# Kernel tuning notes

Measured on AMD Instinct MI355X. Metric: run time of the kernel, lower is better.

## Reference

```python
import jax, jax.numpy as jnp
import numpy as np

D_MODEL = 256
N_HEAD = 8


def quick_gelu(x):
    return x * jax.nn.sigmoid(1.702 * x)


def setup_inputs() -> dict:
    key = jax.random.key(0)
    ks = jax.random.split(key, 7)
    d = D_MODEL
    s = 0.02
    return {
        "x": jax.random.normal(ks[0], (2, 512, d), dtype=jnp.float32),
        "W_qkv": jax.random.normal(ks[1], (d, 3 * d), dtype=jnp.float32) * s,
        "b_qkv": jnp.zeros((3 * d,), dtype=jnp.float32),
        "W_fc": jax.random.normal(ks[2], (d, 4 * d), dtype=jnp.float32) * s,
        "b_fc": jnp.zeros((4 * d,), dtype=jnp.float32),
        "W_proj": jax.random.normal(ks[3], (4 * d, d), dtype=jnp.float32) * s,
        "b_proj": jnp.zeros((d,), dtype=jnp.float32),
    }


def attention_l1(x, W_qkv, b_qkv):
    bs, n_ctx, width = x.shape
    h = N_HEAD
    c = width // h
    scale = 1.0 / jnp.sqrt(jnp.asarray(c, x.dtype))
    qkv = (x @ W_qkv + b_qkv).reshape(bs, n_ctx, h, 3 * c)
    q, k, v = jnp.split(qkv, 3, axis=-1)  # each (b, t, h, c)
    qh = q.transpose(0, 2, 1, 3)  # (b, h, t, c)
    kh = k.transpose(0, 2, 1, 3)  # (b, h, s, c)
    vh = v.transpose(0, 2, 1, 3)  # (b, h, s, c)
    # L1 distance: sum_c |q - k| * scale  -> (b, h, t, s)
    dist = jnp.sum(jnp.abs(qh[:, :, :, None, :] - kh[:, :, None, :, :]), axis=-1) * scale
    weight = 1.0 / (0.001 + dist)
    idx = jnp.arange(n_ctx)
    weight = weight.at[:, :, idx, idx].set(0.0)
    wdtype = weight.dtype
    weight = jax.nn.softmax(weight.astype(jnp.float32), axis=-1).astype(wdtype)
    out = jnp.einsum('bhts,bhsc->bthc', weight, vh)
    return out.reshape(bs, n_ctx, width)


def reference(x, W_qkv, b_qkv, W_fc, b_fc, W_proj, b_proj):
    x = x + attention_l1(x, W_qkv, b_qkv)
    h = quick_gelu(x @ W_fc + b_fc)
    x = x + (h @ W_proj + b_proj)
    return x
```

## Files before the change

kernel.cpp:

```cpp
#include <hip/hip_runtime.h>
#include <hip/hip_bf16.h>
#include <hip/hip_fp16.h>

#define DM   256
#define NH   8
#define HC   32
#define SEQ  512
#define MTOT 1024

#define B_X1   0
#define B_QH   (1u<<20)
#define B_KH   0x180000u
#define B_VT   0x200000u
#define B_WFCT 0x280000u
#define B_WPJT 0x300000u

typedef __attribute__((ext_vector_type(8))) __bf16 bf16x8;
typedef __attribute__((ext_vector_type(4))) __bf16 bf16x4;
typedef __attribute__((ext_vector_type(4))) float  f32x4;

__device__ __forceinline__ float qgelu(float x) {
    return x / (1.0f + __expf(-1.702f * x));
}

__global__ __launch_bounds__(256)
void qkv_k(const float* __restrict__ x, const float* __restrict__ W,
           const float* __restrict__ bias,
           const float* __restrict__ Wfc, const float* __restrict__ Wproj,
           char* __restrict__ wsb)
{
    __shared__ float lt[64 * 65];
    const int bid = blockIdx.x, tid = threadIdx.x;

    if (bid >= 768) {
        const int tt = bid - 768;
        const float* src; __bf16* dst; int K, N, tile;
        if (tt < 64) { src = Wfc;   dst = (__bf16*)(wsb + B_WFCT); K = 256;  N = 1024; tile = tt; }
        else         { src = Wproj; dst = (__bf16*)(wsb + B_WPJT); K = 1024; N = 256;  tile = tt - 64; }
        const int nn = N >> 6;
        const int k0 = (tile / nn) * 64, n0 = (tile % nn) * 64;
        const int rr0 = tid >> 4, c4 = tid & 15;
        #pragma unroll
        for (int i = 0; i < 4; ++i) {
            const int rr = rr0 + i * 16;
            float4 v = *(const float4*)&src[(size_t)(k0 + rr) * N + n0 + c4 * 4];
            lt[rr * 65 + c4 * 4 + 0] = v.x; lt[rr * 65 + c4 * 4 + 1] = v.y;
            lt[rr * 65 + c4 * 4 + 2] = v.z; lt[rr * 65 + c4 * 4 + 3] = v.w;
        }
        __syncthreads();
        #pragma unroll
        for (int i = 0; i < 4; ++i) {
            const int rr = rr0 + i * 16;
            bf16x4 b;
            b.x = (__bf16)lt[(c4 * 4 + 0) * 65 + rr];
            b.y = (__bf16)lt[(c4 * 4 + 1) * 65 + rr];
            b.z = (__bf16)lt[(c4 * 4 + 2) * 65 + rr];
            b.w = (__bf16)lt[(c4 * 4 + 3) * 65 + rr];
            *(bf16x4*)&dst[(size_t)(n0 + rr) * K + k0 + c4 * 4] = b;
        }
        return;
    }

    const int lane = tid & 63, wv = tid >> 6;
    const int widx = bid * 4 + wv;
    const int m0 = (widx & 63) * 16, n0 = (widx >> 6) * 16;
    const int r = lane & 15, q = lane >> 4;

    const float* ap = x + (size_t)(m0 + r) * DM + q * 8;
    const float* bp = W + (size_t)(q * 8) * 768 + n0 + r;

    f32x4 acc = {0.f, 0.f, 0.f, 0.f};
    #pragma unroll
    for (int kt = 0; kt < DM; kt += 32) {
        float4 a0 = *(const float4*)(ap + kt);
        float4 a1 = *(const float4*)(ap + kt + 4);
        bf16x8 af;
        af[0] = (__bf16)a0.x; af[1] = (__bf16)a0.y; af[2] = (__bf16)a0.z; af[3] = (__bf16)a0.w;
        af[4] = (__bf16)a1.x; af[5] = (__bf16)a1.y; af[6] = (__bf16)a1.z; af[7] = (__bf16)a1.w;
        bf16x8 bf;
        #pragma unroll
        for (int j = 0; j < 8; ++j)
            bf[j] = (__bf16)bp[(size_t)(kt + j) * 768];
        acc = __builtin_amdgcn_mfma_f32_16x16x32_bf16(af, bf, acc, 0, 0, 0);
    }

    __half*  qh  = (__half*)(wsb + B_QH);
    __half*  kh  = (__half*)(wsb + B_KH);
    __bf16*  vtb = (__bf16*)(wsb + B_VT);
    const int n = n0 + r;
    const float bn = bias[n];
    const int h = n / 96, jj = n % 96;
    #pragma unroll
    for (int i = 0; i < 4; ++i) {
        const int m = m0 + q * 4 + i;
        const float v = acc[i] + bn;
        const int b = m >> 9, t = m & 511;
        const int bh = b * NH + h;
        if (jj < 32)      qh[((size_t)(bh * SEQ + t)) * HC + jj]        = (__half)v;
        else if (jj < 64) kh[((size_t)(bh * SEQ + t)) * HC + (jj - 32)] = (__half)v;
        else              vtb[((size_t)(bh * HC + (jj - 64))) * SEQ + t] = (__bf16)v;
    }
}

#define QT 16
#define PSTRIDE 514

__global__ __launch_bounds__(512, 4)
void attn_k(const char* __restrict__ wsb, const float* __restrict__ xin,
            float* __restrict__ x1, const float* __restrict__ bproj,
            float* __restrict__ out)
{
    __shared__ __half2 qtile[QT * 16];
    __shared__ __bf16  pmat[QT * PSTRIDE];
    __shared__ float   psum[QT * 8];
    __shared__ float   pinv[QT];

    const __half*  qhg = (const __half*)(wsb + B_QH);
    const __half*  khg = (const __half*)(wsb + B_KH);
    const __bf16*  vtb = (const __bf16*)(wsb + B_VT);

    const int tid  = threadIdx.x;
    const int lane = tid & 63;
    const int wv   = tid >> 6;
    const int sg   = tid;
    const int bh   = blockIdx.x >> 5;
    const int qbase = (blockIdx.x & 31) * QT;
    const float scale = 0.17677669529663687f;

    const __half2* kp = (const __half2*)(khg + ((size_t)(bh * SEQ + sg)) * HC);
    __half2 kr[16];
    #pragma unroll
    for (int j = 0; j < 16; ++j) kr[j] = kp[j];

    if (tid < 256) {
        const int t = tid >> 4, j = tid & 15;
        qtile[t * 16 + j] =
            *(const __half2*)(qhg + ((size_t)(bh * SEQ + qbase + t)) * HC + j * 2);
    }
    __syncthreads();

    #pragma unroll 4
    for (int t = 0; t < QT; ++t) {
        __half2 acc2 = __floats2half2_rn(0.f, 0.f);
        #pragma unroll
        for (int j = 0; j < 16; ++j) {
            __half2 dif = __hsub2(kr[j], qtile[t * 16 + j]);
            unsigned u = (*(unsigned*)&dif) & 0x7FFF7FFFu;
            acc2 = __hadd2(acc2, *(__half2*)&u);
        }
        const float d = __low2float(acc2) + __high2float(acc2);
        float w = 1.0f / (0.001f + d * scale);
        if (sg == qbase + t) w = 0.0f;
        float p = __expf(w);
        float se = p;
        #pragma unroll
        for (int off = 32; off >= 1; off >>= 1) se += __shfl_xor(se, off, 64);
        pmat[t * PSTRIDE + sg] = (__bf16)p;
        if (lane == 0) psum[t * 8 + wv] = se;
    }
    __syncthreads();

    if (tid < QT) {
        float s = 0.f;
        #pragma unroll
        for (int j = 0; j < 8; ++j) s += psum[tid * 8 + j];
        pinv[tid] = 1.0f / s;
    }
    __syncthreads();

    if (wv < 2) {
        const int r = lane & 15, q = lane >> 4;
        const __bf16* bp  = vtb + ((size_t)(bh * HC + wv * 16 + r)) * SEQ + q * 8;
        const __bf16* apm = &pmat[r * PSTRIDE + q * 8];
        f32x4 acc = {0.f, 0.f, 0.f, 0.f};
        #pragma unroll
        for (int kt = 0; kt < SEQ; kt += 32) {
            bf16x8 af = *(const bf16x8*)(apm + kt);
            bf16x8 bf = *(const bf16x8*)(bp + kt);
            acc = __builtin_amdgcn_mfma_f32_16x16x32_bf16(af, bf, acc, 0, 0, 0);
        }
        const int b = bh >> 3, hh = bh & 7;
        const int c = wv * 16 + r;
        const int col = hh * HC + c;
        const float bpn = bproj[col];
        #pragma unroll
        for (int i = 0; i < 4; ++i) {
            const int tl = q * 4 + i;
            const int t  = qbase + tl;
            const float v = acc[i] * pinv[tl];
            const int idx = ((b * SEQ + t) * DM) + col;
            const float res = xin[idx] + v;
            x1[idx]  = res;
            out[idx] = res + bpn;
        }
    }
}

#define HSTR 264

__global__ __launch_bounds__(256)
void mlp_k(const float* __restrict__ X1, const char* __restrict__ wsb,
           const float* __restrict__ bfc, float* __restrict__ out)
{
    __shared__ __bf16 hs[16 * HSTR];
    const __bf16* Wf = (const __bf16*)(wsb + B_WFCT);
    const __bf16* Wp = (const __bf16*)(wsb + B_WPJT);

    const int tid  = threadIdx.x;
    const int lane = tid & 63;
    const int wv   = tid >> 6;
    const int mt   = blockIdx.x & 63;
    const int ns   = blockIdx.x >> 6;
    const int m0   = mt * 16;
    const int r    = lane & 15, q = lane >> 4;

    {
        const float* ap = X1 + (size_t)(m0 + r) * DM + q * 8;
        f32x4 acc[4] = {};
        #pragma unroll
        for (int kt = 0; kt < DM; kt += 32) {
            float4 a0 = *(const float4*)(ap + kt);
            float4 a1 = *(const float4*)(ap + kt + 4);
            bf16x8 af;
            af[0] = (__bf16)a0.x; af[1] = (__bf16)a0.y; af[2] = (__bf16)a0.z; af[3] = (__bf16)a0.w;
            af[4] = (__bf16)a1.x; af[5] = (__bf16)a1.y; af[6] = (__bf16)a1.z; af[7] = (__bf16)a1.w;
            #pragma unroll
            for (int nt = 0; nt < 4; ++nt) {
                const int n0 = ns * 256 + (wv * 4 + nt) * 16;
                bf16x8 bf = *(const bf16x8*)(Wf + (size_t)(n0 + r) * DM + q * 8 + kt);
                acc[nt] = __builtin_amdgcn_mfma_f32_16x16x32_bf16(af, bf, acc[nt], 0, 0, 0);
            }
        }
        #pragma unroll
        for (int nt = 0; nt < 4; ++nt) {
            const int nl = (wv * 4 + nt) * 16 + r;
            const float bn = bfc[ns * 256 + nl];
            #pragma unroll
            for (int i = 0; i < 4; ++i)
                hs[(q * 4 + i) * HSTR + nl] = (__bf16)qgelu(acc[nt][i] + bn);
        }
    }
    __syncthreads();

    {
        f32x4 acc[4] = {};
        const __bf16* al = &hs[r * HSTR + q * 8];
        #pragma unroll
        for (int kt = 0; kt < 256; kt += 32) {
            bf16x8 af = *(const bf16x8*)(al + kt);
            #pragma unroll
            for (int nt = 0; nt < 4; ++nt) {
                const int n0 = wv * 64 + nt * 16;
                bf16x8 bf = *(const bf16x8*)(Wp + (size_t)(n0 + r) * 1024 +
                                             ns * 256 + q * 8 + kt);
                acc[nt] = __builtin_amdgcn_mfma_f32_16x16x32_bf16(af, bf, acc[nt], 0, 0, 0);
            }
        }
        #pragma unroll
        for (int nt = 0; nt < 4; ++nt) {
            const int n = wv * 64 + nt * 16 + r;
            #pragma unroll
            for (int i = 0; i < 4; ++i) {
                const int m = m0 + q * 4 + i;
                atomicAdd(&out[(size_t)m * DM + n], acc[nt][i]);
            }
        }
    }
}

extern "C" void kernel_launch(void* const* d_in, const int* in_sizes, int n_in,
                              void* d_out, int out_size, void* d_ws, size_t ws_size,
                              hipStream_t stream)
{
    (void)in_sizes; (void)n_in; (void)out_size; (void)ws_size;
    const float* x     = (const float*)d_in[0];
    const float* Wqkv  = (const float*)d_in[1];
    const float* bqkv  = (const float*)d_in[2];
    const float* Wfc   = (const float*)d_in[3];
    const float* bfc   = (const float*)d_in[4];
    const float* Wproj = (const float*)d_in[5];
    const float* bproj = (const float*)d_in[6];
    float* out = (float*)d_out;
    char*  wsb = (char*)d_ws;
    float* x1  = (float*)(wsb + B_X1);

    qkv_k<<<896, 256, 0, stream>>>(x, Wqkv, bqkv, Wfc, Wproj, wsb);

    attn_k<<<512, 512, 0, stream>>>(wsb, x, x1, bproj, out);

    mlp_k<<<256, 256, 0, stream>>>(x1, wsb, bfc, out);
}
```

Before: 106.3 us.

## Move weight transposes into attention kernel, store x1 as bf16, split L1 accumulators

Moves the Wfc/Wproj fp32-to-bf16 transpose blocks out of the QKV kernel and into extra blocks of the attention launch, so the conversion overlaps attention work instead of lengthening the QKV pass. The residual x1 is now written as bf16, which halves that write and the MLP's read and removes the in-kernel conversion. The L1 distance loop uses two independent half2 accumulators to shorten the dependency chain. Attention launch bounds drop from 4 to 2 blocks per CU, and the added 16.6KB lt buffer raises shared memory per block, so occupancy and register allocation may change.

```diff
diff --git a/kernel.cpp b/kernel.cpp
--- a/kernel.cpp
+++ b/kernel.cpp
@@ -8,7 +8,7 @@
 #define SEQ  512
 #define MTOT 1024
 
-#define B_X1   0
+#define B_X1B  0
 #define B_QH   (1u<<20)
 #define B_KH   0x180000u
 #define B_VT   0x200000u
@@ -25,44 +25,11 @@
 
 __global__ __launch_bounds__(256)
 void qkv_k(const float* __restrict__ x, const float* __restrict__ W,
-           const float* __restrict__ bias,
-           const float* __restrict__ Wfc, const float* __restrict__ Wproj,
-           char* __restrict__ wsb)
-{
-    __shared__ float lt[64 * 65];
-    const int bid = blockIdx.x, tid = threadIdx.x;
-
-    if (bid >= 768) {
-        const int tt = bid - 768;
-        const float* src; __bf16* dst; int K, N, tile;
-        if (tt < 64) { src = Wfc;   dst = (__bf16*)(wsb + B_WFCT); K = 256;  N = 1024; tile = tt; }
-        else         { src = Wproj; dst = (__bf16*)(wsb + B_WPJT); K = 1024; N = 256;  tile = tt - 64; }
-        const int nn = N >> 6;
-        const int k0 = (tile / nn) * 64, n0 = (tile % nn) * 64;
-        const int rr0 = tid >> 4, c4 = tid & 15;
-        #pragma unroll
-        for (int i = 0; i < 4; ++i) {
-            const int rr = rr0 + i * 16;
-            float4 v = *(const float4*)&src[(size_t)(k0 + rr) * N + n0 + c4 * 4];
-            lt[rr * 65 + c4 * 4 + 0] = v.x; lt[rr * 65 + c4 * 4 + 1] = v.y;
-            lt[rr * 65 + c4 * 4 + 2] = v.z; lt[rr * 65 + c4 * 4 + 3] = v.w;
-        }
-        __syncthreads();
-        #pragma unroll
-        for (int i = 0; i < 4; ++i) {
-            const int rr = rr0 + i * 16;
-            bf16x4 b;
-            b.x = (__bf16)lt[(c4 * 4 + 0) * 65 + rr];
-            b.y = (__bf16)lt[(c4 * 4 + 1) * 65 + rr];
-            b.z = (__bf16)lt[(c4 * 4 + 2) * 65 + rr];
-            b.w = (__bf16)lt[(c4 * 4 + 3) * 65 + rr];
-            *(bf16x4*)&dst[(size_t)(n0 + rr) * K + k0 + c4 * 4] = b;
-        }
-        return;
-    }
-
+           const float* __restrict__ bias, char* __restrict__ wsb)
+{
+    const int tid = threadIdx.x;
     const int lane = tid & 63, wv = tid >> 6;
-    const int widx = bid * 4 + wv;
+    const int widx = blockIdx.x * 4 + wv;
     const int m0 = (widx & 63) * 16, n0 = (widx >> 6) * 16;
     const int r = lane & 15, q = lane >> 4;
 
@@ -105,21 +72,56 @@
 #define QT 16
 #define PSTRIDE 514
 
-__global__ __launch_bounds__(512, 4)
-void attn_k(const char* __restrict__ wsb, const float* __restrict__ xin,
-            float* __restrict__ x1, const float* __restrict__ bproj,
-            float* __restrict__ out)
+__global__ __launch_bounds__(512, 2)
+void attn_k(const char* __restrict__ wsb_c, const float* __restrict__ xin,
+            const float* __restrict__ bproj, float* __restrict__ out,
+            const float* __restrict__ Wfc, const float* __restrict__ Wproj)
 {
     __shared__ __half2 qtile[QT * 16];
     __shared__ __bf16  pmat[QT * PSTRIDE];
     __shared__ float   psum[QT * 8];
     __shared__ float   pinv[QT];
+    __shared__ float   lt[64 * 65];
+
+    char* wsb = (char*)wsb_c;
+    const int tid = threadIdx.x;
+
+    if (blockIdx.x >= 512) {
+        const int tt = blockIdx.x - 512;
+        const float* src; __bf16* dst; int K, N, tile;
+        if (tt < 64) { src = Wfc;   dst = (__bf16*)(wsb + B_WFCT); K = 256;  N = 1024; tile = tt; }
+        else         { src = Wproj; dst = (__bf16*)(wsb + B_WPJT); K = 1024; N = 256;  tile = tt - 64; }
+        const int nn = N >> 6;
+        const int k0 = (tile / nn) * 64, n0 = (tile % nn) * 64;
+        const int rr = tid >> 3;
+        const int c4 = (tid & 7) * 2;
+        #pragma unroll
+        for (int p = 0; p < 2; ++p) {
+            float4 v = *(const float4*)&src[(size_t)(k0 + rr) * N + n0 + (c4 + p) * 4];
+            lt[rr * 65 + (c4 + p) * 4 + 0] = v.x;
+            lt[rr * 65 + (c4 + p) * 4 + 1] = v.y;
+            lt[rr * 65 + (c4 + p) * 4 + 2] = v.z;
+            lt[rr * 65 + (c4 + p) * 4 + 3] = v.w;
+        }
+        __syncthreads();
+        #pragma unroll
+        for (int p = 0; p < 2; ++p) {
+            const int kc = (c4 + p) * 4;
+            bf16x4 b;
+            b.x = (__bf16)lt[(kc + 0) * 65 + rr];
+            b.y = (__bf16)lt[(kc + 1) * 65 + rr];
+            b.z = (__bf16)lt[(kc + 2) * 65 + rr];
+            b.w = (__bf16)lt[(kc + 3) * 65 + rr];
+            *(bf16x4*)&dst[(size_t)(n0 + rr) * K + k0 + kc] = b;
+        }
+        return;
+    }
 
     const __half*  qhg = (const __half*)(wsb + B_QH);
     const __half*  khg = (const __half*)(wsb + B_KH);
     const __bf16*  vtb = (const __bf16*)(wsb + B_VT);
-
-    const int tid  = threadIdx.x;
+    __bf16*        x1b = (__bf16*)(wsb + B_X1B);
+
     const int lane = tid & 63;
     const int wv   = tid >> 6;
     const int sg   = tid;
@@ -141,13 +143,17 @@
 
     #pragma unroll 4
     for (int t = 0; t < QT; ++t) {
-        __half2 acc2 = __floats2half2_rn(0.f, 0.f);
-        #pragma unroll
-        for (int j = 0; j < 16; ++j) {
-            __half2 dif = __hsub2(kr[j], qtile[t * 16 + j]);
-            unsigned u = (*(unsigned*)&dif) & 0x7FFF7FFFu;
-            acc2 = __hadd2(acc2, *(__half2*)&u);
-        }
+        __half2 a0 = __floats2half2_rn(0.f, 0.f), a1 = a0;
+        #pragma unroll
+        for (int j = 0; j < 16; j += 2) {
+            __half2 d0 = __hsub2(kr[j],   qtile[t * 16 + j]);
+            __half2 d1 = __hsub2(kr[j+1], qtile[t * 16 + j + 1]);
+            unsigned u0 = (*(unsigned*)&d0) & 0x7FFF7FFFu;
+            unsigned u1 = (*(unsigned*)&d1) & 0x7FFF7FFFu;
+            a0 = __hadd2(a0, *(__half2*)&u0);
+            a1 = __hadd2(a1, *(__half2*)&u1);
+        }
+        __half2 acc2 = __hadd2(a0, a1);
         const float d = __low2float(acc2) + __high2float(acc2);
         float w = 1.0f / (0.001f + d * scale);
         if (sg == qbase + t) w = 0.0f;
@@ -190,7 +196,7 @@
             const float v = acc[i] * pinv[tl];
             const int idx = ((b * SEQ + t) * DM) + col;
             const float res = xin[idx] + v;
-            x1[idx]  = res;
+            x1b[idx] = (__bf16)res;
             out[idx] = res + bpn;
         }
     }
@@ -199,12 +205,13 @@
 #define HSTR 264
 
 __global__ __launch_bounds__(256)
-void mlp_k(const float* __restrict__ X1, const char* __restrict__ wsb,
-           const float* __restrict__ bfc, float* __restrict__ out)
+void mlp_k(const char* __restrict__ wsb, const float* __restrict__ bfc,
+           float* __restrict__ out)
 {
     __shared__ __bf16 hs[16 * HSTR];
-    const __bf16* Wf = (const __bf16*)(wsb + B_WFCT);
-    const __bf16* Wp = (const __bf16*)(wsb + B_WPJT);
+    const __bf16* X1B = (const __bf16*)(wsb + B_X1B);
+    const __bf16* Wf  = (const __bf16*)(wsb + B_WFCT);
+    const __bf16* Wp  = (const __bf16*)(wsb + B_WPJT);
 
     const int tid  = threadIdx.x;
     const int lane = tid & 63;
@@ -215,15 +222,11 @@
     const int r    = lane & 15, q = lane >> 4;
 
     {
-        const float* ap = X1 + (size_t)(m0 + r) * DM + q * 8;
+        const __bf16* ap = X1B + (size_t)(m0 + r) * DM + q * 8;
         f32x4 acc[4] = {};
         #pragma unroll
         for (int kt = 0; kt < DM; kt += 32) {
-            float4 a0 = *(const float4*)(ap + kt);
-            float4 a1 = *(const float4*)(ap + kt + 4);
-            bf16x8 af;
-            af[0] = (__bf16)a0.x; af[1] = (__bf16)a0.y; af[2] = (__bf16)a0.z; af[3] = (__bf16)a0.w;
-            af[4] = (__bf16)a1.x; af[5] = (__bf16)a1.y; af[6] = (__bf16)a1.z; af[7] = (__bf16)a1.w;
+            bf16x8 af = *(const bf16x8*)(ap + kt);
             #pragma unroll
             for (int nt = 0; nt < 4; ++nt) {
                 const int n0 = ns * 256 + (wv * 4 + nt) * 16;
@@ -282,11 +285,10 @@
     const float* bproj = (const float*)d_in[6];
     float* out = (float*)d_out;
     char*  wsb = (char*)d_ws;
-    float* x1  = (float*)(wsb + B_X1);
-
-    qkv_k<<<896, 256, 0, stream>>>(x, Wqkv, bqkv, Wfc, Wproj, wsb);
-
-    attn_k<<<512, 512, 0, stream>>>(wsb, x, x1, bproj, out);
-
-    mlp_k<<<256, 256, 0, stream>>>(x1, wsb, bfc, out);
-}
+
+    qkv_k<<<768, 256, 0, stream>>>(x, Wqkv, bqkv, wsb);
+
+    attn_k<<<640, 512, 0, stream>>>(wsb, x, bproj, out, Wfc, Wproj);
+
+    mlp_k<<<256, 256, 0, stream>>>(wsb, bfc, out);
+}
```

New measurement: 106.8 us. Within noise of the previous version (+0.5%).

## Fuse attention and MLP kernels with global counter barrier and bf16 x1

Applied to the files above, without the earlier changes.

Merges the attention and MLP launches into one grid of 768 blocks. The last 256 blocks spin on a global atomic counter until all 512 attention blocks have published their results. The intermediate x1 is now stored as bf16, which halves its traffic, and the MLP blocks move to 512 threads, each wave handling 2 N-tiles instead of 4. The aim is to drop one launch gap and overlap the MLP startup. The cost is that spinning blocks hold CU slots, there is a deadlock risk if the attention blocks cannot all become resident, the bounded spin loop can exit early, and the launch bounds drop to 2 blocks per CU.

```diff
diff --git a/kernel.cpp b/kernel.cpp
--- a/kernel.cpp
+++ b/kernel.cpp
@@ -8,12 +8,13 @@
 #define SEQ  512
 #define MTOT 1024
 
-#define B_X1   0
+#define B_X1B  0
 #define B_QH   (1u<<20)
 #define B_KH   0x180000u
 #define B_VT   0x200000u
 #define B_WFCT 0x280000u
 #define B_WPJT 0x300000u
+#define B_CTR  0x380000u
 
 typedef __attribute__((ext_vector_type(8))) __bf16 bf16x8;
 typedef __attribute__((ext_vector_type(4))) __bf16 bf16x4;
@@ -31,6 +32,8 @@
 {
     __shared__ float lt[64 * 65];
     const int bid = blockIdx.x, tid = threadIdx.x;
+
+    if (bid == 0 && tid == 0) *(unsigned*)(wsb + B_CTR) = 0u;
 
     if (bid >= 768) {
         const int tt = bid - 768;
@@ -104,136 +107,151 @@
 
 #define QT 16
 #define PSTRIDE 514
-
-__global__ __launch_bounds__(512, 4)
-void attn_k(const char* __restrict__ wsb, const float* __restrict__ xin,
-            float* __restrict__ x1, const float* __restrict__ bproj,
-            float* __restrict__ out)
+#define HSTR 264
+
+__global__ __launch_bounds__(512, 2)
+void attn_mlp_k(char* __restrict__ wsb, const float* __restrict__ xin,
+                const float* __restrict__ bproj, const float* __restrict__ bfc,
+                float* __restrict__ out)
 {
-    __shared__ __half2 qtile[QT * 16];
-    __shared__ __bf16  pmat[QT * PSTRIDE];
-    __shared__ float   psum[QT * 8];
-    __shared__ float   pinv[QT];
-
-    const __half*  qhg = (const __half*)(wsb + B_QH);
-    const __half*  khg = (const __half*)(wsb + B_KH);
-    const __bf16*  vtb = (const __bf16*)(wsb + B_VT);
-
-    const int tid  = threadIdx.x;
+    __shared__ __align__(16) char smem[18048];
+    unsigned* ctr = (unsigned*)(wsb + B_CTR);
+    const int tid = threadIdx.x;
     const int lane = tid & 63;
     const int wv   = tid >> 6;
-    const int sg   = tid;
-    const int bh   = blockIdx.x >> 5;
-    const int qbase = (blockIdx.x & 31) * QT;
-    const float scale = 0.17677669529663687f;
-
-    const __half2* kp = (const __half2*)(khg + ((size_t)(bh * SEQ + sg)) * HC);
-    __half2 kr[16];
-    #pragma unroll
-    for (int j = 0; j < 16; ++j) kr[j] = kp[j];
-
-    if (tid < 256) {
-        const int t = tid >> 4, j = tid & 15;
-        qtile[t * 16 + j] =
-            *(const __half2*)(qhg + ((size_t)(bh * SEQ + qbase + t)) * HC + j * 2);
+
+    if (blockIdx.x < 512) {
+        __bf16*  pmat  = (__bf16*)smem;
+        __half2* qtile = (__half2*)(smem + 16448);
+        float*   psum  = (float*)(smem + 17472);
+        float*   pinv  = (float*)(smem + 17984);
+
+        const __half* qhg = (const __half*)(wsb + B_QH);
+        const __half* khg = (const __half*)(wsb + B_KH);
+        const __bf16* vtb = (const __bf16*)(wsb + B_VT);
+        __bf16*       x1b = (__bf16*)(wsb + B_X1B);
+
+        const int sg   = tid;
+        const int bh   = blockIdx.x >> 5;
+        const int qbase = (blockIdx.x & 31) * QT;
+        const float scale = 0.17677669529663687f;
+
+        const __half2* kp = (const __half2*)(khg + ((size_t)(bh * SEQ + sg)) * HC);
+        __half2 kr[16];
+        #pragma unroll
+        for (int j = 0; j < 16; ++j) kr[j] = kp[j];
+
+        if (tid < 256) {
+            const int t = tid >> 4, j = tid & 15;
+            qtile[t * 16 + j] =
+                *(const __half2*)(qhg + ((size_t)(bh * SEQ + qbase + t)) * HC + j * 2);
+        }
+        __syncthreads();
+
+        #pragma unroll 4
+        for (int t = 0; t < QT; ++t) {
+            __half2 a0 = __floats2half2_rn(0.f, 0.f), a1 = a0;
+            #pragma unroll
+            for (int j = 0; j < 16; j += 2) {
+                __half2 d0 = __hsub2(kr[j],   qtile[t * 16 + j]);
+                __half2 d1 = __hsub2(kr[j+1], qtile[t * 16 + j + 1]);
+                unsigned u0 = (*(unsigned*)&d0) & 0x7FFF7FFFu;
+                unsigned u1 = (*(unsigned*)&d1) & 0x7FFF7FFFu;
+                a0 = __hadd2(a0, *(__half2*)&u0);
+                a1 = __hadd2(a1, *(__half2*)&u1);
+            }
+            __half2 acc2 = __hadd2(a0, a1);
+            const float d = __low2float(acc2) + __high2float(acc2);
+            float w = 1.0f / (0.001f + d * scale);
+            if (sg == qbase + t) w = 0.0f;
+            float p = __expf(w);
+            float se = p;
+            #pragma unroll
+            for (int off = 32; off >= 1; off >>= 1) se += __shfl_xor(se, off, 64);
+            pmat[t * PSTRIDE + sg] = (__bf16)p;
+            if (lane == 0) psum[t * 8 + wv] = se;
+        }
+        __syncthreads();
+
+        if (tid < QT) {
+            float s = 0.f;
+            #pragma unroll
+            for (int j = 0; j < 8; ++j) s += psum[tid * 8 + j];
+            pinv[tid] = 1.0f / s;
+        }
+        __syncthreads();
+
+        if (wv < 2) {
+            const int r = lane & 15, q = lane >> 4;
+            const __bf16* bp  = vtb + ((size_t)(bh * HC + wv * 16 + r)) * SEQ + q * 8;
+            const __bf16* apm = &pmat[r * PSTRIDE + q * 8];
+            f32x4 acc = {0.f, 0.f, 0.f, 0.f};
+            #pragma unroll
+            for (int kt = 0; kt < SEQ; kt += 32) {
+                bf16x8 af = *(const bf16x8*)(apm + kt);
+                bf16x8 bf = *(const bf16x8*)(bp + kt);
+                acc = __builtin_amdgcn_mfma_f32_16x16x32_bf16(af, bf, acc, 0, 0, 0);
+            }
+            const int b = bh >> 3, hh = bh & 7;
+            const int c = wv * 16 + r;
+            const int col = hh * HC + c;
+            const float bpn = bproj[col];
+            #pragma unroll
+            for (int i = 0; i < 4; ++i) {
+                const int tl = q * 4 + i;
+                const int t  = qbase + tl;
+                const float v = acc[i] * pinv[tl];
+                const int idx = ((b * SEQ + t) * DM) + col;
+                const float res = xin[idx] + v;
+                x1b[idx] = (__bf16)res;
+                out[idx] = res + bpn;
+            }
+        }
+
+        __threadfence();
+        __syncthreads();
+        if (tid == 0)
+            __hip_atomic_fetch_add(ctr, 1u, __ATOMIC_RELEASE, __HIP_MEMORY_SCOPE_AGENT);
+        return;
+    }
+
+    if (tid == 0) {
+        unsigned it = 0;
+        while (__hip_atomic_load(ctr, __ATOMIC_ACQUIRE, __HIP_MEMORY_SCOPE_AGENT) < 512u) {
+            __builtin_amdgcn_s_sleep(16);
+            if (++it > (1u << 24)) break;
+        }
     }
     __syncthreads();
-
-    #pragma unroll 4
-    for (int t = 0; t < QT; ++t) {
-        __half2 acc2 = __floats2half2_rn(0.f, 0.f);
-        #pragma unroll
-        for (int j = 0; j < 16; ++j) {
-            __half2 dif = __hsub2(kr[j], qtile[t * 16 + j]);
-            unsigned u = (*(unsigned*)&dif) & 0x7FFF7FFFu;
-            acc2 = __hadd2(acc2, *(__half2*)&u);
-        }
-        const float d = __low2float(acc2) + __high2float(acc2);
-        float w = 1.0f / (0.001f + d * scale);
-        if (sg == qbase + t) w = 0.0f;
-        float p = __expf(w);
-        float se = p;
-        #pragma unroll
-        for (int off = 32; off >= 1; off >>= 1) se += __shfl_xor(se, off, 64);
-        pmat[t * PSTRIDE + sg] = (__bf16)p;
-        if (lane == 0) psum[t * 8 + wv] = se;
-    }
-    __syncthreads();
-
-    if (tid < QT) {
-        float s = 0.f;
-        #pragma unroll
-        for (int j = 0; j < 8; ++j) s += psum[tid * 8 + j];
-        pinv[tid] = 1.0f / s;
-    }
-    __syncthreads();
-
-    if (wv < 2) {
-        const int r = lane & 15, q = lane >> 4;
-        const __bf16* bp  = vtb + ((size_t)(bh * HC + wv * 16 + r)) * SEQ + q * 8;
-        const __bf16* apm = &pmat[r * PSTRIDE + q * 8];
-        f32x4 acc = {0.f, 0.f, 0.f, 0.f};
-        #pragma unroll
-        for (int kt = 0; kt < SEQ; kt += 32) {
-            bf16x8 af = *(const bf16x8*)(apm + kt);
-            bf16x8 bf = *(const bf16x8*)(bp + kt);
-            acc = __builtin_amdgcn_mfma_f32_16x16x32_bf16(af, bf, acc, 0, 0, 0);
-        }
-        const int b = bh >> 3, hh = bh & 7;
-        const int c = wv * 16 + r;
-        const int col = hh * HC + c;
-        const float bpn = bproj[col];
-        #pragma unroll
-        for (int i = 0; i < 4; ++i) {
-            const int tl = q * 4 + i;
-            const int t  = qbase + tl;
-            const float v = acc[i] * pinv[tl];
-            const int idx = ((b * SEQ + t) * DM) + col;
-            const float res = xin[idx] + v;
-            x1[idx]  = res;
-            out[idx] = res + bpn;
-        }
-    }
-}
-
-#define HSTR 264
-
-__global__ __launch_bounds__(256)
-void mlp_k(const float* __restrict__ X1, const char* __restrict__ wsb,
-           const float* __restrict__ bfc, float* __restrict__ out)
-{
-    __shared__ __bf16 hs[16 * HSTR];
-    const __bf16* Wf = (const __bf16*)(wsb + B_WFCT);
-    const __bf16* Wp = (const __bf16*)(wsb + B_WPJT);
-
-    const int tid  = threadIdx.x;
-    const int lane = tid & 63;
-    const int wv   = tid >> 6;
-    const int mt   = blockIdx.x & 63;
-    const int ns   = blockIdx.x >> 6;
+    __threadfence();
+
+    __bf16* hs = (__bf16*)smem;
+    const __bf16* X1B = (const __bf16*)(wsb + B_X1B);
+    const __bf16* Wf  = (const __bf16*)(wsb + B_WFCT);
+    const __bf16* Wp  = (const __bf16*)(wsb + B_WPJT);
+
+    const int bid2 = blockIdx.x - 512;
+    const int mt   = bid2 & 63;
+    const int ns   = bid2 >> 6;
     const int m0   = mt * 16;
     const int r    = lane & 15, q = lane >> 4;
 
     {
-        const float* ap = X1 + (size_t)(m0 + r) * DM + q * 8;
-        f32x4 acc[4] = {};
+        const __bf16* ap = X1B + (size_t)(m0 + r) * DM + q * 8;
+        f32x4 acc[2] = {};
         #pragma unroll
         for (int kt = 0; kt < DM; kt += 32) {
-            float4 a0 = *(const float4*)(ap + kt);
-            float4 a1 = *(const float4*)(ap + kt + 4);
-            bf16x8 af;
-            af[0] = (__bf16)a0.x; af[1] = (__bf16)a0.y; af[2] = (__bf16)a0.z; af[3] = (__bf16)a0.w;
-            af[4] = (__bf16)a1.x; af[5] = (__bf16)a1.y; af[6] = (__bf16)a1.z; af[7] = (__bf16)a1.w;
-            #pragma unroll
-            for (int nt = 0; nt < 4; ++nt) {
-                const int n0 = ns * 256 + (wv * 4 + nt) * 16;
-                bf16x8 bf = *(const bf16x8*)(Wf + (size_t)(n0 + r) * DM + q * 8 + kt);
+            bf16x8 af = *(const bf16x8*)(ap + kt);
+            #pragma unroll
+            for (int nt = 0; nt < 2; ++nt) {
+                const int n0g = ns * 256 + (wv * 2 + nt) * 16;
+                bf16x8 bf = *(const bf16x8*)(Wf + (size_t)(n0g + r) * DM + q * 8 + kt);
                 acc[nt] = __builtin_amdgcn_mfma_f32_16x16x32_bf16(af, bf, acc[nt], 0, 0, 0);
             }
         }
         #pragma unroll
-        for (int nt = 0; nt < 4; ++nt) {
-            const int nl = (wv * 4 + nt) * 16 + r;
+        for (int nt = 0; nt < 2; ++nt) {
+            const int nl = (wv * 2 + nt) * 16 + r;
             const float bn = bfc[ns * 256 + nl];
             #pragma unroll
             for (int i = 0; i < 4; ++i)
@@ -243,22 +261,22 @@
     __syncthreads();
 
     {
-        f32x4 acc[4] = {};
+        f32x4 acc[2] = {};
         const __bf16* al = &hs[r * HSTR + q * 8];
         #pragma unroll
         for (int kt = 0; kt < 256; kt += 32) {
             bf16x8 af = *(const bf16x8*)(al + kt);
             #pragma unroll
-            for (int nt = 0; nt < 4; ++nt) {
-                const int n0 = wv * 64 + nt * 16;
+            for (int nt = 0; nt < 2; ++nt) {
+                const int n0 = (wv * 2 + nt) * 16;
                 bf16x8 bf = *(const bf16x8*)(Wp + (size_t)(n0 + r) * 1024 +
                                              ns * 256 + q * 8 + kt);
                 acc[nt] = __builtin_amdgcn_mfma_f32_16x16x32_bf16(af, bf, acc[nt], 0, 0, 0);
             }
         }
         #pragma unroll
-        for (int nt = 0; nt < 4; ++nt) {
-            const int n = wv * 64 + nt * 16 + r;
+        for (int nt = 0; nt < 2; ++nt) {
+            const int n = (wv * 2 + nt) * 16 + r;
             #pragma unroll
             for (int i = 0; i < 4; ++i) {
                 const int m = m0 + q * 4 + i;
@@ -282,11 +300,8 @@
     const float* bproj = (const float*)d_in[6];
     float* out = (float*)d_out;
     char*  wsb = (char*)d_ws;
-    float* x1  = (float*)(wsb + B_X1);
 
     qkv_k<<<896, 256, 0, stream>>>(x, Wqkv, bqkv, Wfc, Wproj, wsb);
 
-    attn_k<<<512, 512, 0, stream>>>(wsb, x, x1, bproj, out);
-
-    mlp_k<<<256, 256, 0, stream>>>(x1, wsb, bfc, out);
+    attn_mlp_k<<<768, 512, 0, stream>>>(wsb, x, bproj, bfc, out);
 }
```

After: 245.7 us. 131% more time.
